# Kernel optimization log

Hardware: AMD Instinct MI355X
Metric: run time of the kernel (lower is better)

The kernel has to match this reference:

```python
import jax, jax.numpy as jnp
import numpy as np
import math

NUM_HEADS = 16
D_MODEL = 1024
LN_EPS = 1e-5


def _layer_norm(x, g, b):
    mu = jnp.mean(x, axis=-1, keepdims=True)
    var = jnp.mean((x - mu) ** 2, axis=-1, keepdims=True)
    return (x - mu) / jnp.sqrt(var + LN_EPS) * g + b


def setup_inputs() -> dict:
    key = jax.random.key(0)
    ks = jax.random.split(key, 12)
    B, H, W, d = 32, 16, 16, D_MODEL
    P, F = 64, 128
    s = 0.02
    return {
        "x": jax.random.normal(ks[0], (B, H, W, d), jnp.float32),
        "pattern_features": jax.random.normal(ks[1], (B, P, F), jnp.float32),
        "wq": jax.random.normal(ks[2], (d, d), jnp.float32) * s,
        "bq": jnp.zeros((d,), jnp.float32),
        "wk": jax.random.normal(ks[3], (d, d), jnp.float32) * s,
        "bk": jnp.zeros((d,), jnp.float32),
        "wv": jax.random.normal(ks[4], (d, d), jnp.float32) * s,
        "bv": jnp.zeros((d,), jnp.float32),
        "wo": jax.random.normal(ks[5], (d, d), jnp.float32) * s,
        "bo": jnp.zeros((d,), jnp.float32),
        "ln_g": jnp.ones((d,), jnp.float32),
        "ln_b": jnp.zeros((d,), jnp.float32),
    }


def reference(x, pattern_features, wq, bq, wk, bk, wv, bv, wo, bo, ln_g, ln_b):
    B, H, W, d = x.shape
    S = H * W
    nh = NUM_HEADS
    dk = d // nh
    x_seq = x.reshape(B, S, d)

    def proj(w, b):
        return (x_seq @ w.T + b).reshape(B, S, nh, dk).transpose(0, 2, 1, 3)  # (B,nh,S,dk)

    q, k, v = proj(wq, bq), proj(wk, bk), proj(wv, bv)
    scores = jnp.einsum("bhsd,bhtd->bhst", q, k) / math.sqrt(dk)  # (B,nh,S,S)

    # creative bias: diversity bonus on top-left min(S,64) block, same for all heads
    m = min(S, 64)
    sim = jnp.einsum("bpf,bqf->bpq", pattern_features, pattern_features)
    div = 1.0 - jax.nn.softmax(sim, axis=-1)  # (B,P,P)
    bias = jnp.zeros((B, nh, S, S), x.dtype)
    bias = bias.at[:, :, :m, :m].set(div[:, None, :m, :m] * 0.1)

    # faithful to torch: scores + bias.unsqueeze(0) -> rank-5 (1,B,nh,S,S)
    scores5 = scores[None] + bias[None]
    aw = jax.nn.softmax(scores5, axis=-1)
    attn = jnp.matmul(aw, v)  # (1,B,nh,S,dk) via broadcasting
    # faithful to torch transpose(1,2).view(B,S,d): row-major reshape of (1,nh,B,S,dk)
    attn = jnp.transpose(attn, (0, 2, 1, 3, 4)).reshape(B, S, d)

    out = attn @ wo.T + bo
    out = _layer_norm(out + x_seq, ln_g, ln_b)

    attention_weights = jax.nn.softmax(scores, axis=-1).mean(axis=1)  # (B,S,S)
    return out.reshape(B, H, W, d), attention_weights
```

## Files before the change

kernel.cpp:

```cpp
#include <hip/hip_runtime.h>

typedef unsigned short u16;
typedef unsigned int   u32;
typedef short bf16x8 __attribute__((ext_vector_type(8)));
typedef float f32x4  __attribute__((ext_vector_type(4)));

__device__ __forceinline__ float bf2f(u16 u){
  union { u32 u; float f; } c; c.u = ((u32)u) << 16; return c.f;
}
__device__ __forceinline__ u16 f2bf(float f){
  union { float f; u32 u; } c; c.f = f;
  u32 u = c.u + 0x7fffu + ((c.u >> 16) & 1u);
  return (u16)(u >> 16);
}

__device__ __forceinline__ void gload16(const u16* g, u16* l){
  __builtin_amdgcn_global_load_lds((const __attribute__((address_space(1))) u32*)g,
                                   (__attribute__((address_space(3))) u32*)l, 16, 0, 0);
}

__device__ __forceinline__ float waveRed(float v, int ismax){
  #pragma unroll
  for (int o = 32; o > 0; o >>= 1){
    float t = __shfl_xor(v, o, 64);
    v = ismax ? fmaxf(v, t) : (v + t);
  }
  return v;
}
__device__ __forceinline__ float blockRed(float v, int ismax, float* red, int tid){
  v = waveRed(v, ismax);
  __syncthreads();
  if ((tid & 63) == 0) red[tid >> 6] = v;
  __syncthreads();
  return ismax ? fmaxf(fmaxf(red[0], red[1]), fmaxf(red[2], red[3]))
               : (red[0] + red[1] + red[2] + red[3]);
}

__global__ __launch_bounds__(256)
void conv_x(const float* __restrict__ src, u16* __restrict__ dst){
  const size_t i = ((size_t)blockIdx.x * 256 + threadIdx.x) * 8;
  const float4 a = *(const float4*)(src + i);
  const float4 b = *(const float4*)(src + i + 4);
  uint4 o;
  o.x = (u32)f2bf(a.x) | ((u32)f2bf(a.y) << 16);
  o.y = (u32)f2bf(a.z) | ((u32)f2bf(a.w) << 16);
  o.z = (u32)f2bf(b.x) | ((u32)f2bf(b.y) << 16);
  o.w = (u32)f2bf(b.z) | ((u32)f2bf(b.w) << 16);
  *(uint4*)(dst + i) = o;
}

__global__ __launch_bounds__(256)
void conv_w4(const float* __restrict__ w0, const float* __restrict__ w1,
             const float* __restrict__ w2, const float* __restrict__ w3,
             u16* __restrict__ dst){
  const float* s = blockIdx.y == 0 ? w0 : (blockIdx.y == 1 ? w1 : (blockIdx.y == 2 ? w2 : w3));
  u16* d = dst + (size_t)blockIdx.y * 1048576;
  const size_t i = ((size_t)blockIdx.x * 256 + threadIdx.x) * 8;
  const float4 a = *(const float4*)(s + i);
  const float4 b = *(const float4*)(s + i + 4);
  uint4 o;
  o.x = (u32)f2bf(a.x) | ((u32)f2bf(a.y) << 16);
  o.y = (u32)f2bf(a.z) | ((u32)f2bf(a.w) << 16);
  o.z = (u32)f2bf(b.x) | ((u32)f2bf(b.y) << 16);
  o.w = (u32)f2bf(b.z) | ((u32)f2bf(b.w) << 16);
  *(uint4*)(d + i) = o;
}

__global__ __launch_bounds__(256)
void div_kernel(const float* __restrict__ pf, float* __restrict__ divp)
{
  __shared__ float pfs[64][129];
  __shared__ float svs[64][65];
  const int b = blockIdx.x;
  const int tid = threadIdx.x;
  const float* pb = pf + (size_t)b * 8192;
  for (int i = tid; i < 8192; i += 256) pfs[i >> 7][i & 127] = pb[i];
  __syncthreads();
  const int p = tid & 63, qg = tid >> 6;
  for (int qq = qg * 16; qq < qg * 16 + 16; ++qq){
    float a = 0.f;
    #pragma unroll 8
    for (int f = 0; f < 128; ++f) a += pfs[p][f] * pfs[qq][f];
    svs[p][qq] = a;
  }
  __syncthreads();
  if (tid < 64){
    float m = -1e30f;
    for (int qq = 0; qq < 64; ++qq) m = fmaxf(m, svs[tid][qq]);
    float s = 0.f;
    for (int qq = 0; qq < 64; ++qq){ const float e = __expf(svs[tid][qq] - m); svs[tid][qq] = e; s += e; }
    const float inv = 1.f / s;
    float* dr = divp + ((size_t)b * 64 + tid) * 64;
    for (int qq = 0; qq < 64; ++qq) dr[qq] = 0.1f * (1.f - svs[tid][qq] * inv);
  }
}

template<int MODE>
__global__ __launch_bounds__(256)
void gemm_lds(const u16* __restrict__ A, const u16* __restrict__ Wb,
              const float* __restrict__ bias0, const float* __restrict__ bias1,
              const float* __restrict__ bias2, void* __restrict__ outp)
{
  __shared__ u16 As[128 * 32];
  __shared__ u16 Bs[128 * 32];
  const int tid = threadIdx.x, lane = tid & 63, w = tid >> 6;
  const int wm = (w >> 1) * 64, wn = (w & 1) * 64;
  const int bm = blockIdx.x;
  int bn = blockIdx.y;
  const u16* Wp = Wb;
  const float* bias = bias0;
  float scale = 1.f;
  int wsel = 0;
  if (MODE == 0){
    wsel = bn >> 3; bn &= 7;
    Wp = Wb + (size_t)wsel * 1048576;
    bias = wsel == 0 ? bias0 : (wsel == 1 ? bias1 : bias2);
    if (wsel == 0) scale = 0.125f;
  }

  const f32x4 z = {0.f, 0.f, 0.f, 0.f};
  f32x4 acc[4][4];
  #pragma unroll
  for (int i = 0; i < 4; ++i)
    #pragma unroll
    for (int j = 0; j < 4; ++j) acc[i][j] = z;

  const int r4 = lane >> 2, c8 = (lane & 3) * 8;
  const int ca0 = w * 2, ca1 = w * 2 + 1;
  const u16* ga0 = A  + (size_t)(bm * 128 + ca0 * 16 + r4) * 1024 + c8;
  const u16* ga1 = A  + (size_t)(bm * 128 + ca1 * 16 + r4) * 1024 + c8;
  const u16* gb0 = Wp + (size_t)(bn * 128 + ca0 * 16 + r4) * 1024 + c8;
  const u16* gb1 = Wp + (size_t)(bn * 128 + ca1 * 16 + r4) * 1024 + c8;
  u16* la0 = As + ca0 * 512 + lane * 8;
  u16* la1 = As + ca1 * 512 + lane * 8;
  u16* lb0 = Bs + ca0 * 512 + lane * 8;
  u16* lb1 = Bs + ca1 * 512 + lane * 8;

  const int fr = lane & 15, q8 = (lane >> 4) * 8;
  for (int k0 = 0; k0 < 1024; k0 += 32){
    __syncthreads();
    gload16(ga0 + k0, la0);
    gload16(ga1 + k0, la1);
    gload16(gb0 + k0, lb0);
    gload16(gb1 + k0, lb1);
    __syncthreads();
    bf16x8 af[4], bfv[4];
    #pragma unroll
    for (int i = 0; i < 4; ++i) af[i]  = *(const bf16x8*)&As[(wm + i * 16 + fr) * 32 + q8];
    #pragma unroll
    for (int j = 0; j < 4; ++j) bfv[j] = *(const bf16x8*)&Bs[(wn + j * 16 + fr) * 32 + q8];
    #pragma unroll
    for (int i = 0; i < 4; ++i)
      #pragma unroll
      for (int j = 0; j < 4; ++j)
        acc[i][j] = __builtin_amdgcn_mfma_f32_16x16x32_bf16(af[i], bfv[j], acc[i][j], 0, 0, 0);
  }

  #pragma unroll
  for (int i = 0; i < 4; ++i){
    #pragma unroll
    for (int j = 0; j < 4; ++j){
      const int gr0 = bm * 128 + wm + i * 16 + ((lane >> 4) * 4);
      const int gc  = bn * 128 + wn + j * 16 + (lane & 15);
      const float bvv = bias[gc];
      #pragma unroll
      for (int r = 0; r < 4; ++r){
        const int gr = gr0 + r;
        const float val = (acc[i][j][r] + bvv) * scale;
        if (MODE == 0){
          const int b = gr >> 8, s = gr & 255, h = gc >> 6, kk = gc & 63;
          ((u16*)outp)[(size_t)wsel * 8388608 + (size_t)b * 262144 +
                       (size_t)h * 16384 + (size_t)s * 64 + kk] = f2bf(val);
        } else {
          ((float*)outp)[(size_t)gr * 1024 + gc] = val;
        }
      }
    }
  }
}

__global__ __launch_bounds__(256)
void attn_mfma(const u16* __restrict__ q, const u16* __restrict__ k,
               const u16* __restrict__ v, const float* __restrict__ divp,
               u16* __restrict__ attn_s)
{
  __shared__ u16 Vt[64][264];
  __shared__ u16 Ps[4][16][136];
  const int blk = blockIdx.x;
  const int bh = blk >> 2, rq = blk & 3;
  const int b = bh >> 4, h = bh & 15;
  const int tid = threadIdx.x, lane = tid & 63, w = tid >> 6;
  const int quad = lane >> 4, l15 = lane & 15;
  const u16* kh = k + (size_t)bh * 16384;
  const u16* vh = v + (size_t)bh * 16384;
  const u16* qh = q + (size_t)bh * 16384;

  #pragma unroll
  for (int c = 0; c < 4; ++c){
    const int pidx = tid + c * 256;
    const int t2 = pidx & 127;
    const int n0 = (pidx >> 7) * 8;
    const uint4 a  = *(const uint4*)(vh + (2 * t2) * 64 + n0);
    const uint4 bb = *(const uint4*)(vh + (2 * t2 + 1) * 64 + n0);
    const u32 aa[4] = {a.x, a.y, a.z, a.w};
    const u32 bb4[4] = {bb.x, bb.y, bb.z, bb.w};
    #pragma unroll
    for (int j2 = 0; j2 < 4; ++j2){
      const u32 lo = aa[j2], hi = bb4[j2];
      *(u32*)&Vt[n0 + 2 * j2    ][2 * t2] = (lo & 0xffffu) | (hi << 16);
      *(u32*)&Vt[n0 + 2 * j2 + 1][2 * t2] = (lo >> 16) | (hi & 0xffff0000u);
    }
  }
  __syncthreads();

  const f32x4 z = {0.f, 0.f, 0.f, 0.f};
  const int bp = 2 * h + (b >> 4);
  const int row0 = rq * 64 + w * 16;
  const bf16x8 af0 = *(const bf16x8*)(qh + (size_t)(row0 + l15) * 64 + quad * 8);
  const bf16x8 af1 = *(const bf16x8*)(qh + (size_t)(row0 + l15) * 64 + 32 + quad * 8);
  f32x4 sc[16];
  #pragma unroll
  for (int ct = 0; ct < 16; ++ct){
    const bf16x8 b0 = *(const bf16x8*)(kh + (size_t)(ct * 16 + l15) * 64 + quad * 8);
    const bf16x8 b1 = *(const bf16x8*)(kh + (size_t)(ct * 16 + l15) * 64 + 32 + quad * 8);
    f32x4 a = __builtin_amdgcn_mfma_f32_16x16x32_bf16(af0, b0, z, 0, 0, 0);
    sc[ct]  = __builtin_amdgcn_mfma_f32_16x16x32_bf16(af1, b1, a, 0, 0, 0);
  }
  if (rq == 0){
    const float* dv = divp + (size_t)b * 4096 + (size_t)(w * 16 + quad * 4) * 64 + l15;
    #pragma unroll
    for (int ct = 0; ct < 4; ++ct)
      #pragma unroll
      for (int rr = 0; rr < 4; ++rr)
        sc[ct][rr] += dv[rr * 64 + ct * 16];
  }
  float rs[4];
  #pragma unroll
  for (int rr = 0; rr < 4; ++rr){
    float m = sc[0][rr];
    #pragma unroll
    for (int ct = 1; ct < 16; ++ct) m = fmaxf(m, sc[ct][rr]);
    #pragma unroll
    for (int o = 1; o < 16; o <<= 1) m = fmaxf(m, __shfl_xor(m, o, 64));
    float s = 0.f;
    #pragma unroll
    for (int ct = 0; ct < 16; ++ct){
      const float e = __expf(sc[ct][rr] - m); sc[ct][rr] = e; s += e;
    }
    #pragma unroll
    for (int o = 1; o < 16; o <<= 1) s += __shfl_xor(s, o, 64);
    rs[rr] = 1.f / s;
  }
  f32x4 o4[4] = {z, z, z, z};
  #pragma unroll
  for (int half = 0; half < 2; ++half){
    #pragma unroll
    for (int ct = 0; ct < 8; ++ct)
      #pragma unroll
      for (int rr = 0; rr < 4; ++rr)
        Ps[w][quad * 4 + rr][ct * 16 + l15] = f2bf(sc[half * 8 + ct][rr] * rs[rr]);
    #pragma unroll
    for (int kc = 0; kc < 4; ++kc){
      const bf16x8 pa = *(const bf16x8*)&Ps[w][l15][kc * 32 + quad * 8];
      #pragma unroll
      for (int nt = 0; nt < 4; ++nt){
        const bf16x8 vb8 = *(const bf16x8*)&Vt[nt * 16 + l15][half * 128 + kc * 32 + quad * 8];
        o4[nt] = __builtin_amdgcn_mfma_f32_16x16x32_bf16(pa, vb8, o4[nt], 0, 0, 0);
      }
    }
  }
  const int sp = (b & 15) * 16 + rq * 4 + w;
  #pragma unroll
  for (int nt = 0; nt < 4; ++nt)
    #pragma unroll
    for (int rr = 0; rr < 4; ++rr){
      const int slo = quad * 4 + rr;
      const int cp = slo * 64 + nt * 16 + l15;
      attn_s[((size_t)bp * 256 + sp) * 1024 + cp] = f2bf(o4[nt][rr]);
    }
}

__global__ __launch_bounds__(256)
void aw_kernel(const u16* __restrict__ q, const u16* __restrict__ k,
               float* __restrict__ aw)
{
  __shared__ float Ws[4][16][258];
  const int blk = blockIdx.x;
  const int b = blk >> 4, st = blk & 15;
  const int tid = threadIdx.x, lane = tid & 63, w = tid >> 6;
  const int quad = lane >> 4, l15 = lane & 15;
  const int rowb = st * 16;
  const f32x4 z = {0.f, 0.f, 0.f, 0.f};
  float awacc[16][4] = {};
  #pragma unroll
  for (int hh = 0; hh < 4; ++hh){
    const int h = w * 4 + hh;
    const u16* kh = k + (((size_t)b * 16 + h) * 16384);
    const u16* qh = q + (((size_t)b * 16 + h) * 16384);
    const bf16x8 af0 = *(const bf16x8*)(qh + (size_t)(rowb + l15) * 64 + quad * 8);
    const bf16x8 af1 = *(const bf16x8*)(qh + (size_t)(rowb + l15) * 64 + 32 + quad * 8);
    f32x4 sc[16];
    #pragma unroll
    for (int ct = 0; ct < 16; ++ct){
      const bf16x8 b0 = *(const bf16x8*)(kh + (size_t)(ct * 16 + l15) * 64 + quad * 8);
      const bf16x8 b1 = *(const bf16x8*)(kh + (size_t)(ct * 16 + l15) * 64 + 32 + quad * 8);
      f32x4 a = __builtin_amdgcn_mfma_f32_16x16x32_bf16(af0, b0, z, 0, 0, 0);
      sc[ct]  = __builtin_amdgcn_mfma_f32_16x16x32_bf16(af1, b1, a, 0, 0, 0);
    }
    #pragma unroll
    for (int rr = 0; rr < 4; ++rr){
      float m = sc[0][rr];
      #pragma unroll
      for (int ct = 1; ct < 16; ++ct) m = fmaxf(m, sc[ct][rr]);
      #pragma unroll
      for (int o = 1; o < 16; o <<= 1) m = fmaxf(m, __shfl_xor(m, o, 64));
      float s = 0.f;
      #pragma unroll
      for (int ct = 0; ct < 16; ++ct){
        const float e = __expf(sc[ct][rr] - m); sc[ct][rr] = e; s += e;
      }
      #pragma unroll
      for (int o = 1; o < 16; o <<= 1) s += __shfl_xor(s, o, 64);
      const float inv = 1.f / s;
      #pragma unroll
      for (int ct = 0; ct < 16; ++ct) awacc[ct][rr] += sc[ct][rr] * inv;
    }
  }
  #pragma unroll
  for (int ct = 0; ct < 16; ++ct)
    #pragma unroll
    for (int rr = 0; rr < 4; ++rr)
      Ws[w][quad * 4 + rr][ct * 16 + l15] = awacc[ct][rr];
  __syncthreads();
  float* dst = aw + (size_t)b * 65536 + (size_t)rowb * 256;
  for (int t = tid; t < 4096; t += 256){
    const int r = t >> 8, c = t & 255;
    dst[(size_t)r * 256 + c] =
        (Ws[0][r][c] + Ws[1][r][c] + Ws[2][r][c] + Ws[3][r][c]) * 0.0625f;
  }
}

__global__ __launch_bounds__(256)
void ln_kernel(const float* __restrict__ y2, const float* __restrict__ x,
               const float* __restrict__ g, const float* __restrict__ bb,
               float* __restrict__ outp)
{
  __shared__ float red[4];
  const int r = blockIdx.x, tid = threadIdx.x;
  const float4 yv = ((const float4*)(y2 + (size_t)r * 1024))[tid];
  const float4 xv = ((const float4*)(x  + (size_t)r * 1024))[tid];
  const float v0 = yv.x + xv.x;
  const float v1 = yv.y + xv.y;
  const float v2 = yv.z + xv.z;
  const float v3 = yv.w + xv.w;
  const float ssum = blockRed(v0 + v1 + v2 + v3, 0, red, tid);
  const float mu = ssum * (1.f / 1024.f);
  const float d0 = v0 - mu, d1 = v1 - mu, d2 = v2 - mu, d3 = v3 - mu;
  const float sq = blockRed(d0 * d0 + d1 * d1 + d2 * d2 + d3 * d3, 0, red, tid);
  const float rstd = rsqrtf(sq * (1.f / 1024.f) + 1e-5f);
  const float4 gv = ((const float4*)g)[tid];
  const float4 bv = ((const float4*)bb)[tid];
  float4 o;
  o.x = d0 * rstd * gv.x + bv.x;
  o.y = d1 * rstd * gv.y + bv.y;
  o.z = d2 * rstd * gv.z + bv.z;
  o.w = d3 * rstd * gv.w + bv.w;
  ((float4*)(outp + (size_t)r * 1024))[tid] = o;
}

extern "C" void kernel_launch(void* const* d_in, const int* in_sizes, int n_in,
                              void* d_out, int out_size, void* d_ws, size_t ws_size,
                              hipStream_t stream)
{
  int ix = -1, ipf = -1, iw[4] = {-1,-1,-1,-1}, iv[6] = {-1,-1,-1,-1,-1,-1};
  int nw = 0, nv = 0;
  for (int i = 0; i < n_in; ++i){
    const int sz = in_sizes[i];
    if (sz == 8388608 && ix < 0) ix = i;
    else if (sz == 262144 && ipf < 0) ipf = i;
    else if (sz == 1048576 && nw < 4) iw[nw++] = i;
    else if (sz == 1024 && nv < 6) iv[nv++] = i;
  }
  if (ix < 0 || ipf < 0 || nw != 4 || nv != 6){
    ix = 0; ipf = 1; iw[0] = 2; iv[0] = 3; iw[1] = 4; iv[1] = 5;
    iw[2] = 6; iv[2] = 7; iw[3] = 8; iv[3] = 9; iv[4] = 10; iv[5] = 11;
  }

  const float* x   = (const float*)d_in[ix];
  const float* pf  = (const float*)d_in[ipf];
  const float* wq  = (const float*)d_in[iw[0]];
  const float* wk  = (const float*)d_in[iw[1]];
  const float* wv  = (const float*)d_in[iw[2]];
  const float* wo  = (const float*)d_in[iw[3]];
  const float* bq  = (const float*)d_in[iv[0]];
  const float* bk  = (const float*)d_in[iv[1]];
  const float* bv  = (const float*)d_in[iv[2]];
  const float* bo  = (const float*)d_in[iv[3]];
  const float* lng = (const float*)d_in[iv[4]];
  const float* lnb = (const float*)d_in[iv[5]];

  float* out0   = (float*)d_out;
  float* aw_out = out0 + 8388608;

  u16* x_bf = (u16*)d_out;
  u16* attn = x_bf + 8388608;
  u16* qkv    = (u16*)d_ws;
  float* divp = (float*)((char*)d_ws + (size_t)48 * 1048576);
  u16* warena = (u16*)((char*)d_ws + (size_t)49 * 1048576);
  float* y2   = (float*)d_ws;

  conv_x<<<4096, 256, 0, stream>>>(x, x_bf);
  conv_w4<<<dim3(512, 4), 256, 0, stream>>>(wq, wk, wv, wo, warena);
  div_kernel<<<32, 256, 0, stream>>>(pf, divp);

  gemm_lds<0><<<dim3(64, 24), 256, 0, stream>>>(x_bf, warena, bq, bk, bv, (void*)qkv);

  u16* qw = qkv, *kw = qkv + 8388608, *vw = qkv + 16777216;
  attn_mfma<<<2048, 256, 0, stream>>>(qw, kw, vw, divp, attn);
  aw_kernel<<<512, 256, 0, stream>>>(qw, kw, aw_out);

  gemm_lds<1><<<dim3(64, 8), 256, 0, stream>>>(attn, warena + 3145728, bo, nullptr, nullptr, (void*)y2);
  ln_kernel<<<8192, 256, 0, stream>>>(y2, x, lng, lnb, out0);
}
```

Before: 338.3 us.

## Fuse prep kernels, deepen GEMM K-tile, reuse V per block in attention

Merges the x/weight bf16 conversion and diversity-bias kernels into one prep launch to cut launch overhead. The GEMM K-step grows from 32 to 64, halving barrier and load-issue rounds at the cost of doubled LDS. Attention now uses one block per (batch, head) that loops over all 256 query rows, so the V transpose into LDS happens once instead of four times, but the grid shrinks to 512 blocks. It also writes paired bf16 outputs via shuffles, and aw_kernel halves its LDS staging buffer by reducing in two chunks, which adds a barrier.

```diff
diff --git a/kernel.cpp b/kernel.cpp
--- a/kernel.cpp
+++ b/kernel.cpp
@@ -37,42 +37,37 @@
 }
 
 __global__ __launch_bounds__(256)
-void conv_x(const float* __restrict__ src, u16* __restrict__ dst){
-  const size_t i = ((size_t)blockIdx.x * 256 + threadIdx.x) * 8;
-  const float4 a = *(const float4*)(src + i);
-  const float4 b = *(const float4*)(src + i + 4);
-  uint4 o;
-  o.x = (u32)f2bf(a.x) | ((u32)f2bf(a.y) << 16);
-  o.y = (u32)f2bf(a.z) | ((u32)f2bf(a.w) << 16);
-  o.z = (u32)f2bf(b.x) | ((u32)f2bf(b.y) << 16);
-  o.w = (u32)f2bf(b.z) | ((u32)f2bf(b.w) << 16);
-  *(uint4*)(dst + i) = o;
-}
-
-__global__ __launch_bounds__(256)
-void conv_w4(const float* __restrict__ w0, const float* __restrict__ w1,
-             const float* __restrict__ w2, const float* __restrict__ w3,
-             u16* __restrict__ dst){
-  const float* s = blockIdx.y == 0 ? w0 : (blockIdx.y == 1 ? w1 : (blockIdx.y == 2 ? w2 : w3));
-  u16* d = dst + (size_t)blockIdx.y * 1048576;
-  const size_t i = ((size_t)blockIdx.x * 256 + threadIdx.x) * 8;
-  const float4 a = *(const float4*)(s + i);
-  const float4 b = *(const float4*)(s + i + 4);
-  uint4 o;
-  o.x = (u32)f2bf(a.x) | ((u32)f2bf(a.y) << 16);
-  o.y = (u32)f2bf(a.z) | ((u32)f2bf(a.w) << 16);
-  o.z = (u32)f2bf(b.x) | ((u32)f2bf(b.y) << 16);
-  o.w = (u32)f2bf(b.z) | ((u32)f2bf(b.w) << 16);
-  *(uint4*)(d + i) = o;
-}
-
-__global__ __launch_bounds__(256)
-void div_kernel(const float* __restrict__ pf, float* __restrict__ divp)
+void prep(const float* __restrict__ x,
+          const float* __restrict__ w0, const float* __restrict__ w1,
+          const float* __restrict__ w2, const float* __restrict__ w3,
+          const float* __restrict__ pf,
+          u16* __restrict__ x_bf, u16* __restrict__ warena,
+          float* __restrict__ divp)
 {
   __shared__ float pfs[64][129];
   __shared__ float svs[64][65];
-  const int b = blockIdx.x;
-  const int tid = threadIdx.x;
+  const int bi = blockIdx.x, tid = threadIdx.x;
+  if (bi < 6144){
+    const float* s; u16* d; size_t i;
+    if (bi < 4096){
+      s = x; d = x_bf; i = ((size_t)bi * 256 + tid) * 8;
+    } else {
+      const int wb = bi - 4096, wi = wb >> 9;
+      s = wi == 0 ? w0 : (wi == 1 ? w1 : (wi == 2 ? w2 : w3));
+      d = warena + (size_t)wi * 1048576;
+      i = ((size_t)(wb & 511) * 256 + tid) * 8;
+    }
+    const float4 a = *(const float4*)(s + i);
+    const float4 b = *(const float4*)(s + i + 4);
+    uint4 o;
+    o.x = (u32)f2bf(a.x) | ((u32)f2bf(a.y) << 16);
+    o.y = (u32)f2bf(a.z) | ((u32)f2bf(a.w) << 16);
+    o.z = (u32)f2bf(b.x) | ((u32)f2bf(b.y) << 16);
+    o.w = (u32)f2bf(b.z) | ((u32)f2bf(b.w) << 16);
+    *(uint4*)(d + i) = o;
+    return;
+  }
+  const int b = bi - 6144;
   const float* pb = pf + (size_t)b * 8192;
   for (int i = tid; i < 8192; i += 256) pfs[i >> 7][i & 127] = pb[i];
   __syncthreads();
@@ -101,8 +96,8 @@
               const float* __restrict__ bias0, const float* __restrict__ bias1,
               const float* __restrict__ bias2, void* __restrict__ outp)
 {
-  __shared__ u16 As[128 * 32];
-  __shared__ u16 Bs[128 * 32];
+  __shared__ u16 As[128 * 64];
+  __shared__ u16 Bs[128 * 64];
   const int tid = threadIdx.x, lane = tid & 63, w = tid >> 6;
   const int wm = (w >> 1) * 64, wn = (w & 1) * 64;
   const int bm = blockIdx.x;
@@ -125,35 +120,39 @@
     #pragma unroll
     for (int j = 0; j < 4; ++j) acc[i][j] = z;
 
-  const int r4 = lane >> 2, c8 = (lane & 3) * 8;
-  const int ca0 = w * 2, ca1 = w * 2 + 1;
-  const u16* ga0 = A  + (size_t)(bm * 128 + ca0 * 16 + r4) * 1024 + c8;
-  const u16* ga1 = A  + (size_t)(bm * 128 + ca1 * 16 + r4) * 1024 + c8;
-  const u16* gb0 = Wp + (size_t)(bn * 128 + ca0 * 16 + r4) * 1024 + c8;
-  const u16* gb1 = Wp + (size_t)(bn * 128 + ca1 * 16 + r4) * 1024 + c8;
-  u16* la0 = As + ca0 * 512 + lane * 8;
-  u16* la1 = As + ca1 * 512 + lane * 8;
-  u16* lb0 = Bs + ca0 * 512 + lane * 8;
-  u16* lb1 = Bs + ca1 * 512 + lane * 8;
+  const int r8 = lane >> 3, c8 = (lane & 7) * 8;
+  const u16* ga[4]; const u16* gb[4]; u16* la[4]; u16* lb[4];
+  #pragma unroll
+  for (int c = 0; c < 4; ++c){
+    const int ca = w * 4 + c;
+    ga[c] = A  + (size_t)(bm * 128 + ca * 8 + r8) * 1024 + c8;
+    gb[c] = Wp + (size_t)(bn * 128 + ca * 8 + r8) * 1024 + c8;
+    la[c] = As + ca * 512 + lane * 8;
+    lb[c] = Bs + ca * 512 + lane * 8;
+  }
 
   const int fr = lane & 15, q8 = (lane >> 4) * 8;
-  for (int k0 = 0; k0 < 1024; k0 += 32){
+  for (int k0 = 0; k0 < 1024; k0 += 64){
     __syncthreads();
-    gload16(ga0 + k0, la0);
-    gload16(ga1 + k0, la1);
-    gload16(gb0 + k0, lb0);
-    gload16(gb1 + k0, lb1);
+    #pragma unroll
+    for (int c = 0; c < 4; ++c){
+      gload16(ga[c] + k0, la[c]);
+      gload16(gb[c] + k0, lb[c]);
+    }
     __syncthreads();
-    bf16x8 af[4], bfv[4];
-    #pragma unroll
-    for (int i = 0; i < 4; ++i) af[i]  = *(const bf16x8*)&As[(wm + i * 16 + fr) * 32 + q8];
-    #pragma unroll
-    for (int j = 0; j < 4; ++j) bfv[j] = *(const bf16x8*)&Bs[(wn + j * 16 + fr) * 32 + q8];
-    #pragma unroll
-    for (int i = 0; i < 4; ++i)
-      #pragma unroll
-      for (int j = 0; j < 4; ++j)
-        acc[i][j] = __builtin_amdgcn_mfma_f32_16x16x32_bf16(af[i], bfv[j], acc[i][j], 0, 0, 0);
+    #pragma unroll
+    for (int s = 0; s < 2; ++s){
+      bf16x8 af[4], bfv[4];
+      #pragma unroll
+      for (int i = 0; i < 4; ++i) af[i]  = *(const bf16x8*)&As[(wm + i * 16 + fr) * 64 + s * 32 + q8];
+      #pragma unroll
+      for (int j = 0; j < 4; ++j) bfv[j] = *(const bf16x8*)&Bs[(wn + j * 16 + fr) * 64 + s * 32 + q8];
+      #pragma unroll
+      for (int i = 0; i < 4; ++i)
+        #pragma unroll
+        for (int j = 0; j < 4; ++j)
+          acc[i][j] = __builtin_amdgcn_mfma_f32_16x16x32_bf16(af[i], bfv[j], acc[i][j], 0, 0, 0);
+    }
   }
 
   #pragma unroll
@@ -186,8 +185,7 @@
 {
   __shared__ u16 Vt[64][264];
   __shared__ u16 Ps[4][16][136];
-  const int blk = blockIdx.x;
-  const int bh = blk >> 2, rq = blk & 3;
+  const int bh = blockIdx.x;
   const int b = bh >> 4, h = bh & 15;
   const int tid = threadIdx.x, lane = tid & 63, w = tid >> 6;
   const int quad = lane >> 4, l15 = lane & 15;
@@ -215,76 +213,88 @@
 
   const f32x4 z = {0.f, 0.f, 0.f, 0.f};
   const int bp = 2 * h + (b >> 4);
-  const int row0 = rq * 64 + w * 16;
-  const bf16x8 af0 = *(const bf16x8*)(qh + (size_t)(row0 + l15) * 64 + quad * 8);
-  const bf16x8 af1 = *(const bf16x8*)(qh + (size_t)(row0 + l15) * 64 + 32 + quad * 8);
-  f32x4 sc[16];
-  #pragma unroll
-  for (int ct = 0; ct < 16; ++ct){
-    const bf16x8 b0 = *(const bf16x8*)(kh + (size_t)(ct * 16 + l15) * 64 + quad * 8);
-    const bf16x8 b1 = *(const bf16x8*)(kh + (size_t)(ct * 16 + l15) * 64 + 32 + quad * 8);
-    f32x4 a = __builtin_amdgcn_mfma_f32_16x16x32_bf16(af0, b0, z, 0, 0, 0);
-    sc[ct]  = __builtin_amdgcn_mfma_f32_16x16x32_bf16(af1, b1, a, 0, 0, 0);
-  }
-  if (rq == 0){
-    const float* dv = divp + (size_t)b * 4096 + (size_t)(w * 16 + quad * 4) * 64 + l15;
-    #pragma unroll
-    for (int ct = 0; ct < 4; ++ct)
-      #pragma unroll
-      for (int rr = 0; rr < 4; ++rr)
-        sc[ct][rr] += dv[rr * 64 + ct * 16];
-  }
-  float rs[4];
-  #pragma unroll
-  for (int rr = 0; rr < 4; ++rr){
-    float m = sc[0][rr];
-    #pragma unroll
-    for (int ct = 1; ct < 16; ++ct) m = fmaxf(m, sc[ct][rr]);
-    #pragma unroll
-    for (int o = 1; o < 16; o <<= 1) m = fmaxf(m, __shfl_xor(m, o, 64));
-    float s = 0.f;
+  const int evn = !(l15 & 1);
+  for (int i = 0; i < 4; ++i){
+    const int row0 = w * 64 + i * 16;
+    const bf16x8 af0 = *(const bf16x8*)(qh + (size_t)(row0 + l15) * 64 + quad * 8);
+    const bf16x8 af1 = *(const bf16x8*)(qh + (size_t)(row0 + l15) * 64 + 32 + quad * 8);
+    f32x4 sc[16];
     #pragma unroll
     for (int ct = 0; ct < 16; ++ct){
-      const float e = __expf(sc[ct][rr] - m); sc[ct][rr] = e; s += e;
-    }
-    #pragma unroll
-    for (int o = 1; o < 16; o <<= 1) s += __shfl_xor(s, o, 64);
-    rs[rr] = 1.f / s;
-  }
-  f32x4 o4[4] = {z, z, z, z};
-  #pragma unroll
-  for (int half = 0; half < 2; ++half){
-    #pragma unroll
-    for (int ct = 0; ct < 8; ++ct)
-      #pragma unroll
-      for (int rr = 0; rr < 4; ++rr)
-        Ps[w][quad * 4 + rr][ct * 16 + l15] = f2bf(sc[half * 8 + ct][rr] * rs[rr]);
-    #pragma unroll
-    for (int kc = 0; kc < 4; ++kc){
-      const bf16x8 pa = *(const bf16x8*)&Ps[w][l15][kc * 32 + quad * 8];
-      #pragma unroll
-      for (int nt = 0; nt < 4; ++nt){
-        const bf16x8 vb8 = *(const bf16x8*)&Vt[nt * 16 + l15][half * 128 + kc * 32 + quad * 8];
-        o4[nt] = __builtin_amdgcn_mfma_f32_16x16x32_bf16(pa, vb8, o4[nt], 0, 0, 0);
+      const bf16x8 b0 = *(const bf16x8*)(kh + (size_t)(ct * 16 + l15) * 64 + quad * 8);
+      const bf16x8 b1 = *(const bf16x8*)(kh + (size_t)(ct * 16 + l15) * 64 + 32 + quad * 8);
+      f32x4 a = __builtin_amdgcn_mfma_f32_16x16x32_bf16(af0, b0, z, 0, 0, 0);
+      sc[ct]  = __builtin_amdgcn_mfma_f32_16x16x32_bf16(af1, b1, a, 0, 0, 0);
+    }
+    if (w == 0){
+      const float* dv = divp + (size_t)b * 4096 + (size_t)(i * 16 + quad * 4) * 64 + l15;
+      #pragma unroll
+      for (int ct = 0; ct < 4; ++ct)
+        #pragma unroll
+        for (int rr = 0; rr < 4; ++rr)
+          sc[ct][rr] += dv[rr * 64 + ct * 16];
+    }
+    float rs[4];
+    #pragma unroll
+    for (int rr = 0; rr < 4; ++rr){
+      float m = sc[0][rr];
+      #pragma unroll
+      for (int ct = 1; ct < 16; ++ct) m = fmaxf(m, sc[ct][rr]);
+      #pragma unroll
+      for (int o = 1; o < 16; o <<= 1) m = fmaxf(m, __shfl_xor(m, o, 64));
+      float s = 0.f;
+      #pragma unroll
+      for (int ct = 0; ct < 16; ++ct){
+        const float e = __expf(sc[ct][rr] - m); sc[ct][rr] = e; s += e;
       }
-    }
-  }
-  const int sp = (b & 15) * 16 + rq * 4 + w;
-  #pragma unroll
-  for (int nt = 0; nt < 4; ++nt)
-    #pragma unroll
-    for (int rr = 0; rr < 4; ++rr){
-      const int slo = quad * 4 + rr;
-      const int cp = slo * 64 + nt * 16 + l15;
-      attn_s[((size_t)bp * 256 + sp) * 1024 + cp] = f2bf(o4[nt][rr]);
-    }
+      #pragma unroll
+      for (int o = 1; o < 16; o <<= 1) s += __shfl_xor(s, o, 64);
+      rs[rr] = 1.f / s;
+    }
+    f32x4 o4[4] = {z, z, z, z};
+    #pragma unroll
+    for (int half = 0; half < 2; ++half){
+      #pragma unroll
+      for (int ct = 0; ct < 8; ++ct)
+        #pragma unroll
+        for (int rr = 0; rr < 4; ++rr){
+          const float vv = sc[half * 8 + ct][rr] * rs[rr];
+          const float ov = __shfl_xor(vv, 1, 64);
+          if (evn)
+            *(u32*)&Ps[w][quad * 4 + rr][ct * 16 + l15] =
+                (u32)f2bf(vv) | ((u32)f2bf(ov) << 16);
+        }
+      #pragma unroll
+      for (int kc = 0; kc < 4; ++kc){
+        const bf16x8 pa = *(const bf16x8*)&Ps[w][l15][kc * 32 + quad * 8];
+        #pragma unroll
+        for (int nt = 0; nt < 4; ++nt){
+          const bf16x8 vb8 = *(const bf16x8*)&Vt[nt * 16 + l15][half * 128 + kc * 32 + quad * 8];
+          o4[nt] = __builtin_amdgcn_mfma_f32_16x16x32_bf16(pa, vb8, o4[nt], 0, 0, 0);
+        }
+      }
+    }
+    const int sp = (b & 15) * 16 + (w * 4 + i);
+    u16* orow = attn_s + ((size_t)bp * 256 + sp) * 1024;
+    #pragma unroll
+    for (int nt = 0; nt < 4; ++nt)
+      #pragma unroll
+      for (int rr = 0; rr < 4; ++rr){
+        const float vv = o4[nt][rr];
+        const float ov = __shfl_xor(vv, 1, 64);
+        if (evn){
+          const int cp = (quad * 4 + rr) * 64 + nt * 16 + l15;
+          *(u32*)(orow + cp) = (u32)f2bf(vv) | ((u32)f2bf(ov) << 16);
+        }
+      }
+  }
 }
 
 __global__ __launch_bounds__(256)
 void aw_kernel(const u16* __restrict__ q, const u16* __restrict__ k,
                float* __restrict__ aw)
 {
-  __shared__ float Ws[4][16][258];
+  __shared__ float Ws[4][16][130];
   const int blk = blockIdx.x;
   const int b = blk >> 4, st = blk & 15;
   const int tid = threadIdx.x, lane = tid & 63, w = tid >> 6;
@@ -326,17 +336,23 @@
       for (int ct = 0; ct < 16; ++ct) awacc[ct][rr] += sc[ct][rr] * inv;
     }
   }
-  #pragma unroll
-  for (int ct = 0; ct < 16; ++ct)
-    #pragma unroll
-    for (int rr = 0; rr < 4; ++rr)
-      Ws[w][quad * 4 + rr][ct * 16 + l15] = awacc[ct][rr];
-  __syncthreads();
   float* dst = aw + (size_t)b * 65536 + (size_t)rowb * 256;
-  for (int t = tid; t < 4096; t += 256){
-    const int r = t >> 8, c = t & 255;
-    dst[(size_t)r * 256 + c] =
-        (Ws[0][r][c] + Ws[1][r][c] + Ws[2][r][c] + Ws[3][r][c]) * 0.0625f;
+  #pragma unroll
+  for (int ch = 0; ch < 2; ++ch){
+    if (ch) __syncthreads();
+    #pragma unroll
+    for (int c2 = 0; c2 < 8; ++c2){
+      const int ct = ch * 8 + c2;
+      #pragma unroll
+      for (int rr = 0; rr < 4; ++rr)
+        Ws[w][quad * 4 + rr][c2 * 16 + l15] = awacc[ct][rr];
+    }
+    __syncthreads();
+    for (int t = tid; t < 2048; t += 256){
+      const int r = t >> 7, c = t & 127;
+      dst[(size_t)r * 256 + ch * 128 + c] =
+          (Ws[0][r][c] + Ws[1][r][c] + Ws[2][r][c] + Ws[3][r][c]) * 0.0625f;
+    }
   }
 }
 
@@ -409,14 +425,12 @@
   u16* warena = (u16*)((char*)d_ws + (size_t)49 * 1048576);
   float* y2   = (float*)d_ws;
 
-  conv_x<<<4096, 256, 0, stream>>>(x, x_bf);
-  conv_w4<<<dim3(512, 4), 256, 0, stream>>>(wq, wk, wv, wo, warena);
-  div_kernel<<<32, 256, 0, stream>>>(pf, divp);
+  prep<<<6176, 256, 0, stream>>>(x, wq, wk, wv, wo, pf, x_bf, warena, divp);
 
   gemm_lds<0><<<dim3(64, 24), 256, 0, stream>>>(x_bf, warena, bq, bk, bv, (void*)qkv);
 
   u16* qw = qkv, *kw = qkv + 8388608, *vw = qkv + 16777216;
-  attn_mfma<<<2048, 256, 0, stream>>>(qw, kw, vw, divp, attn);
+  attn_mfma<<<512, 256, 0, stream>>>(qw, kw, vw, divp, attn);
   aw_kernel<<<512, 256, 0, stream>>>(qw, kw, aw_out);
 
   gemm_lds<1><<<dim3(64, 8), 256, 0, stream>>>(attn, warena + 3145728, bo, nullptr, nullptr, (void*)y2);
```

Result: slower. 389.6 us (+15.2%).
